# Optimization experiments

Measured on AMD Instinct MI355X. Metric: run time of the kernel, lower is better.

The kernel has to match this reference:

```python
import jax, jax.numpy as jnp
import numpy as np

B, S, H, H2, NH, K, L, V, TOUT, MEL = 16, 256, 384, 1536, 2, 3, 4, 256, 1024, 80


def _ln(x, sb):
    # sb: [2, H] -> (scale, bias)
    m = x.mean(-1, keepdims=True)
    v = x.var(-1, keepdims=True)
    return (x - m) * jax.lax.rsqrt(v + 1e-5) * sb[0] + sb[1]


def _conv1d(x, w, b):
    # x: [B, T, Cin], w: [K, Cin, Cout]
    return jax.lax.conv_general_dilated(x, w, (1,), 'SAME',
                                         dimension_numbers=('NWC', 'WIO', 'NWC')) + b


def _mha(x, w, b):
    # w: [4, H, H] (q, k, v, o), b: [4, H]
    T = x.shape[1]
    dh = H // NH
    q = (x @ w[0] + b[0]).reshape(B, T, NH, dh)
    k = (x @ w[1] + b[1]).reshape(B, T, NH, dh)
    v = (x @ w[2] + b[2]).reshape(B, T, NH, dh)
    s = jnp.einsum('bqhd,bkhd->bhqk', q, k) / np.sqrt(dh).astype(np.float32)
    a = jax.nn.softmax(s, axis=-1)
    o = jnp.einsum('bhqk,bkhd->bqhd', a, v).reshape(B, T, H)
    return o @ w[3] + b[3]


def _fft_block(x, aw, ab, c1w, c1b, c2w, c2b, ln):
    x = _ln(x + _mha(x, aw, ab), ln[0])
    f = _conv1d(jax.nn.relu(_conv1d(x, c1w, c1b)), c2w, c2b)
    return _ln(x + f, ln[1])


def _posenc(x):
    T = x.shape[1]
    pos = jnp.arange(T, dtype=jnp.float32)[:, None]
    den = jnp.exp(-np.log(10000.0) * jnp.arange(0, H, 2, dtype=jnp.float32) / H)
    ang = pos * den[None, :]
    pe = jnp.stack([jnp.sin(ang), jnp.cos(ang)], axis=-1).reshape(T, H)
    return x + pe[None]


def setup_inputs() -> dict:
    key = jax.random.key(0)
    ks = iter(jax.random.split(key, 32))
    sc = 0.02
    inp = {}
    inp['tokens'] = jax.random.randint(next(ks), (B, S), 0, V, dtype=jnp.int32)
    inp['alignes'] = jax.random.randint(next(ks), (B, S), 0, 8).astype(jnp.int64)
    inp['tok_emb'] = jax.random.normal(next(ks), (V, H), jnp.float32) * sc
    for pre in ('enc', 'dec'):
        inp[pre + '_attn_w'] = jax.random.normal(next(ks), (L, 4, H, H), jnp.float32) * sc
        inp[pre + '_attn_b'] = jnp.zeros((L, 4, H), jnp.float32)
        inp[pre + '_conv1_w'] = jax.random.normal(next(ks), (L, K, H, H2), jnp.float32) * sc
        inp[pre + '_conv1_b'] = jnp.zeros((L, H2), jnp.float32)
        inp[pre + '_conv2_w'] = jax.random.normal(next(ks), (L, K, H2, H), jnp.float32) * sc
        inp[pre + '_conv2_b'] = jnp.zeros((L, H), jnp.float32)
        ln = jnp.stack([jnp.ones((L, 2, H)), jnp.zeros((L, 2, H))], axis=2)  # [L,2,2,H]
        inp[pre + '_ln'] = ln.astype(jnp.float32)
    inp['al_conv1_w'] = jax.random.normal(next(ks), (K, H, H), jnp.float32) * sc
    inp['al_conv1_b'] = jnp.zeros((H,), jnp.float32)
    inp['al_conv2_w'] = jax.random.normal(next(ks), (K, H, H), jnp.float32) * sc
    inp['al_conv2_b'] = jnp.zeros((H,), jnp.float32)
    inp['al_ln'] = jnp.stack([jnp.ones((2, H)), jnp.zeros((2, H))], axis=1).astype(jnp.float32)
    inp['al_lin_w'] = jax.random.normal(next(ks), (H, 1), jnp.float32) * sc
    inp['al_lin_b'] = jnp.zeros((1,), jnp.float32)
    inp['dec_lin_w'] = jax.random.normal(next(ks), (H, MEL), jnp.float32) * sc
    inp['dec_lin_b'] = jnp.zeros((MEL,), jnp.float32)
    return inp


def reference(tokens, alignes, tok_emb, enc_attn_w, enc_attn_b, enc_conv1_w,
              enc_conv1_b, enc_conv2_w, enc_conv2_b, enc_ln, dec_attn_w,
              dec_attn_b, dec_conv1_w, dec_conv1_b, dec_conv2_w, dec_conv2_b,
              dec_ln, al_conv1_w, al_conv1_b, al_conv2_w, al_conv2_b, al_ln,
              al_lin_w, al_lin_b, dec_lin_w, dec_lin_b):
    # ---- Encoder ----
    x = tok_emb[tokens] * np.sqrt(H).astype(np.float32)
    x = _posenc(x)
    for i in range(L):
        x = _fft_block(x, enc_attn_w[i], enc_attn_b[i], enc_conv1_w[i],
                       enc_conv1_b[i], enc_conv2_w[i], enc_conv2_b[i], enc_ln[i])
    # ---- Aligner (duration predictor) ----
    h = jax.nn.relu(_conv1d(x, al_conv1_w, al_conv1_b))
    h = _ln(h, al_ln[0])
    h = jax.nn.relu(_conv1d(h, al_conv2_w, al_conv2_b))
    h = _ln(h, al_ln[1])
    length_pred = (h @ al_lin_w + al_lin_b)[..., 0]  # [B, S]
    # ---- Length regulator: repeat_interleave + pad_sequence (static TOUT) ----
    dur = alignes.astype(jnp.int32)
    cum = jnp.cumsum(dur, axis=1)                    # [B, S]
    t = jnp.arange(TOUT, dtype=jnp.int32)
    idx = jax.vmap(lambda c: jnp.searchsorted(c, t, side='right'))(cum)  # [B, TOUT]
    valid = t[None, :] < cum[:, -1:]
    idx = jnp.clip(idx, 0, S - 1)
    expanded = jnp.take_along_axis(x, idx[:, :, None], axis=1)
    expanded = expanded * valid[:, :, None].astype(x.dtype)
    # ---- Decoder ----
    y = _posenc(expanded)
    for i in range(L):
        y = _fft_block(y, dec_attn_w[i], dec_attn_b[i], dec_conv1_w[i],
                       dec_conv1_b[i], dec_conv2_w[i], dec_conv2_b[i], dec_ln[i])
    mel = y @ dec_lin_w + dec_lin_b                  # [B, TOUT, 80]
    return jnp.transpose(mel, (0, 2, 1)), length_pred
```

## Files before the change

### kernel.cpp

```cpp
#include <hip/hip_runtime.h>
#include <cstdint>
#include <cstddef>

#define B_    16
#define S_    256
#define H_    384
#define H2_   1536
#define NH_   2
#define DH_   192
#define TOUT_ 1024
#define MEL_  80
#define L_    4

#define F_BIAS  1
#define F_RES   2
#define F_RELU  4
#define F_STF   8
#define F_STB   16
#define F_TRANS 32

typedef __attribute__((ext_vector_type(8))) short short8;
typedef __attribute__((ext_vector_type(4))) float floatx4;

typedef const __attribute__((address_space(1))) unsigned int* as1p;
typedef __attribute__((address_space(3))) unsigned int* as3p;

__device__ __forceinline__ void gld16(const void* g, void* l) {
  __builtin_amdgcn_global_load_lds((as1p)g, (as3p)l, 16, 0, 0);
}

__device__ __forceinline__ short f2b(float f) {
  union { float f; unsigned u; } v; v.f = f;
  unsigned r = (v.u + 0x7fffu + ((v.u >> 16) & 1u)) >> 16;
  return (short)r;
}

__device__ __forceinline__ float pe_val(int t, int i) {
  int j = i >> 1;
  float den = __expf(-9.210340371976184f * (float)(2 * j) / (float)H_);
  float ang = (float)t * den;
  return (i & 1) ? __cosf(ang) : __sinf(ang);
}

__global__ __launch_bounds__(256) void wtrans_kernel(const float* __restrict__ sa,
                                                     const float* __restrict__ sb,
                                                     int na, int K, int N,
                                                     short* __restrict__ dst) {
  __shared__ float t[32][33];
  int id = blockIdx.z;
  const float* s = (id < na) ? sa + (size_t)id * K * N : sb + (size_t)(id - na) * K * N;
  short* o = dst + (size_t)id * K * N;
  int n0 = blockIdx.x * 32, k0 = blockIdx.y * 32;
  int tx = threadIdx.x & 31, ty = threadIdx.x >> 5;
#pragma unroll
  for (int i = 0; i < 4; ++i)
    t[ty + i * 8][tx] = s[(size_t)(k0 + ty + i * 8) * N + n0 + tx];
  __syncthreads();
#pragma unroll
  for (int i = 0; i < 4; ++i)
    o[(size_t)(n0 + ty + i * 8) * K + k0 + tx] = f2b(t[tx][ty + i * 8]);
}

__global__ void melpad_kernel(const float* __restrict__ w, short* __restrict__ dst) {
  int i = blockIdx.x * 256 + threadIdx.x;
  int n = i / H_, k = i - n * H_;
  dst[i] = (n < MEL_) ? f2b(w[(size_t)k * MEL_ + n]) : (short)0;
}

__global__ void embed_kernel(const int* __restrict__ tokens, const float* __restrict__ emb,
                             float* __restrict__ xf, short* __restrict__ xb) {
  int bs = blockIdx.x;
  int t  = bs & (S_ - 1);
  int tok = tokens[bs];
  const float* e = emb + (size_t)tok * H_;
  float* of = xf + (size_t)bs * H_;
  short* ob = xb + (size_t)bs * H_;
  for (int i = threadIdx.x; i < H_; i += blockDim.x) {
    float v = e[i] * 19.595917942265423f + pe_val(t, i);
    of[i] = v; ob[i] = f2b(v);
  }
}

template<int NTAPS, int MTW>
__global__ __launch_bounds__(256) void mfma_gemm(
    const short* __restrict__ A, const short* __restrict__ Wt,
    const float* __restrict__ bias, const float* __restrict__ res,
    float* __restrict__ Cf, short* __restrict__ Cb, const short* __restrict__ zbuf,
    int M, int N, int Kd, int T, int Nout, int flags)
{
  constexpr int TM   = MTW * 32;
  constexpr int HB   = NTAPS / 2;
  constexpr int RA   = TM + NTAPS - 1;
  constexpr int RNDA = (RA + 63) / 64;
  __shared__ __align__(16) short As[RA * 32];
  __shared__ __align__(16) short Bs[NTAPS * 128 * 32];
  const int tid = threadIdx.x;
  const int wave = tid >> 6, lane = tid & 63, quad = lane >> 4, lm = lane & 15;

  const int nbx = gridDim.x;
  const int lin = blockIdx.y * nbx + blockIdx.x;
  const int xcd = lin & 7, j = lin >> 3;
  const int bx = j % nbx;
  const int by = xcd + 8 * (j / nbx);

  const int bm = by * TM, bn = bx * 128;
  const int wm = (wave >> 1) * (TM / 2), wn = (wave & 1) * 64;
  const int b0 = bm / T, t0 = bm - b0 * T;
  floatx4 acc[MTW][4] = {};

  for (int k0 = 0; k0 < Kd; k0 += 32) {
#pragma unroll
    for (int jj = 0; jj < RNDA; ++jj) {
      int r0 = (jj == RNDA - 1) ? (RA - 64) : jj * 64;
      int r = r0 + (tid >> 2);
      int t = t0 - HB + r;
      const short* g = (t >= 0 && t < T)
          ? (A + (size_t)(b0 * T + t) * Kd + k0 + (tid & 3) * 8) : zbuf;
      gld16(g, As + r0 * 32 + wave * 512);
    }
#pragma unroll
    for (int jj = 0; jj < 2 * NTAPS; ++jj) {
      int gi = jj * 256 + tid;
      int tap = gi >> 9, rr = (gi >> 2) & 127, ch = gi & 3;
      const short* g = Wt + ((size_t)tap * N + bn + rr) * Kd + k0 + ch * 8;
      gld16(g, Bs + jj * 2048 + wave * 512);
    }
    __syncthreads();
#pragma unroll
    for (int tap = 0; tap < NTAPS; ++tap) {
      short8 af[MTW], bfr[4];
#pragma unroll
      for (int mt = 0; mt < MTW; ++mt)
        af[mt] = *(const short8*)(&As[(wm + mt * 16 + lm + tap) * 32 + quad * 8]);
#pragma unroll
      for (int nt = 0; nt < 4; ++nt)
        bfr[nt] = *(const short8*)(&Bs[tap * 4096 + (wn + nt * 16 + lm) * 32 + quad * 8]);
#pragma unroll
      for (int mt = 0; mt < MTW; ++mt)
#pragma unroll
        for (int nt = 0; nt < 4; ++nt)
          acc[mt][nt] = __builtin_amdgcn_mfma_f32_16x16x32_bf16(af[mt], bfr[nt],
                                                                acc[mt][nt], 0, 0, 0);
    }
    __syncthreads();
  }

#pragma unroll
  for (int mt = 0; mt < MTW; ++mt) {
#pragma unroll
    for (int r2 = 0; r2 < 4; ++r2) {
      int gm = bm + wm + mt * 16 + quad * 4 + r2;
#pragma unroll
      for (int nt = 0; nt < 4; ++nt) {
        int gn = bn + wn + nt * 16 + lm;
        float v = acc[mt][nt][r2];
        if (flags & F_TRANS) {
          if (gn < Nout) {
            if (flags & F_BIAS) v += bias[gn];
            int bb = gm / T, tt = gm - bb * T;
            Cf[((size_t)bb * Nout + gn) * T + tt] = v;
          }
          continue;
        }
        if (flags & F_BIAS) v += bias[gn];
        size_t idx = (size_t)gm * N + gn;
        if (flags & F_RES) v += res[idx];
        if (flags & F_RELU) v = fmaxf(v, 0.f);
        if (flags & F_STF) Cf[idx] = v;
        if (flags & F_STB) Cb[idx] = f2b(v);
      }
    }
  }
}

__global__ __launch_bounds__(256) void vtrans_kernel(const short* __restrict__ qkv,
                                                     short* __restrict__ vt, int T) {
  __shared__ short tile[32][34];
  int b = blockIdx.z, d0 = blockIdx.y * 32, t0 = blockIdx.x * 32;
  int tx = threadIdx.x & 31, ty = threadIdx.x >> 5;
#pragma unroll
  for (int i = 0; i < 4; ++i)
    tile[ty + i * 8][tx] = qkv[(size_t)(b * T + t0 + ty + i * 8) * 1152 + 768 + d0 + tx];
  __syncthreads();
  int h = (d0 >= DH_) ? 1 : 0;
  int dd0 = d0 - h * DH_;
#pragma unroll
  for (int i = 0; i < 4; ++i)
    vt[((size_t)((b * NH_ + h) * DH_) + dd0 + ty + i * 8) * T + t0 + tx] = tile[tx][ty + i * 8];
}

template<int T>
__global__ __launch_bounds__(256) void attn_flash(const short* __restrict__ qkv,
                                                  const short* __restrict__ vt,
                                                  short* __restrict__ o)
{
  constexpr int NKT = T / 32;
  __shared__ __align__(16) short Kb[2][6144];
  __shared__ __align__(16) short Vb[2][6144];
  __shared__ __align__(16) short Pb[4][16 * 40];
  const int tid = threadIdx.x;
  const int wave = tid >> 6, lane = tid & 63, quad = lane >> 4, lm = lane & 15;
  const int id = blockIdx.x;
  const int bh = id & 31, h = bh & 1, b = bh >> 1;
  const int q0 = (id >> 5) * 64;
  const short* qb = qkv + (size_t)b * T * 1152 + h * DH_;
  const short* kb = qb + 384;
  const short* vb = vt + (size_t)(b * NH_ + h) * DH_ * T;

  short8 qf[6];
  {
    const short* qrow = qb + (size_t)(q0 + wave * 16 + lm) * 1152 + quad * 8;
#pragma unroll
    for (int c6 = 0; c6 < 6; ++c6) qf[c6] = *(const short8*)(qrow + c6 * 32);
  }

  auto stage = [&](int kc, int bi) {
#pragma unroll
    for (int j = 0; j < 3; ++j) {
      int g = j * 256 + tid;
      int lmg = g & 15, qg = (g >> 4) & 3, ct = g >> 6;
      int c6 = ct % 6, kt = ct / 6;
      gld16(kb + (size_t)(kc * 32 + kt * 16 + lmg) * 1152 + c6 * 32 + qg * 8,
            &Kb[bi][j * 2048 + wave * 512]);
    }
#pragma unroll
    for (int j = 0; j < 3; ++j) {
      int g = j * 256 + tid;
      int lmg = g & 15, qg = (g >> 4) & 3, dt = g >> 6;
      gld16(vb + (size_t)(dt * 16 + lmg) * T + kc * 32 + qg * 8,
            &Vb[bi][j * 2048 + wave * 512]);
    }
  };

  float m_r[4] = {-1e30f, -1e30f, -1e30f, -1e30f};
  float l_r[4] = {0.f, 0.f, 0.f, 0.f};
  floatx4 oacc[12] = {};

  stage(0, 0);
  __syncthreads();

  for (int kc = 0; kc < NKT; ++kc) {
    const int cur = kc & 1;
    if (kc + 1 < NKT) stage(kc + 1, cur ^ 1);

    floatx4 s0 = {0.f, 0.f, 0.f, 0.f}, s1 = {0.f, 0.f, 0.f, 0.f};
#pragma unroll
    for (int c6 = 0; c6 < 6; ++c6) {
      short8 k0f = *(const short8*)(&Kb[cur][(c6 * 64 + quad * 16 + lm) * 8]);
      short8 k1f = *(const short8*)(&Kb[cur][((6 + c6) * 64 + quad * 16 + lm) * 8]);
      s0 = __builtin_amdgcn_mfma_f32_16x16x32_bf16(qf[c6], k0f, s0, 0, 0, 0);
      s1 = __builtin_amdgcn_mfma_f32_16x16x32_bf16(qf[c6], k1f, s1, 0, 0, 0);
    }

    float al[4];
#pragma unroll
    for (int r2 = 0; r2 < 4; ++r2) {
      float a = s0[r2] * 0.07216878364870323f;
      float c = s1[r2] * 0.07216878364870323f;
      float t = fmaxf(a, c);
#pragma unroll
      for (int off = 1; off < 16; off <<= 1) t = fmaxf(t, __shfl_xor(t, off, 64));
      float mn = fmaxf(m_r[r2], t);
      al[r2] = __expf(m_r[r2] - mn);
      m_r[r2] = mn;
      float e0 = __expf(a - mn), e1 = __expf(c - mn);
      l_r[r2] = al[r2] * l_r[r2] + e0 + e1;
      Pb[wave][(quad * 4 + r2) * 40 + lm]      = f2b(e0);
      Pb[wave][(quad * 4 + r2) * 40 + 16 + lm] = f2b(e1);
    }
#pragma unroll
    for (int dt = 0; dt < 12; ++dt) {
#pragma unroll
      for (int r2 = 0; r2 < 4; ++r2) oacc[dt][r2] *= al[r2];
    }

    short8 pf = *(const short8*)(&Pb[wave][lm * 40 + quad * 8]);
#pragma unroll
    for (int dt = 0; dt < 12; ++dt) {
      short8 vf = *(const short8*)(&Vb[cur][(dt * 64 + quad * 16 + lm) * 8]);
      oacc[dt] = __builtin_amdgcn_mfma_f32_16x16x32_bf16(pf, vf, oacc[dt], 0, 0, 0);
    }
    __syncthreads();
  }

#pragma unroll
  for (int r2 = 0; r2 < 4; ++r2) {
#pragma unroll
    for (int off = 1; off < 16; off <<= 1) l_r[r2] += __shfl_xor(l_r[r2], off, 64);
    l_r[r2] = 1.f / l_r[r2];
  }
  short* orow = o + (size_t)(b * T + q0 + wave * 16) * H_ + h * DH_;
#pragma unroll
  for (int dt = 0; dt < 12; ++dt) {
#pragma unroll
    for (int r2 = 0; r2 < 4; ++r2)
      orow[(size_t)(quad * 4 + r2) * H_ + dt * 16 + lm] = f2b(oacc[dt][r2] * l_r[r2]);
  }
}

__global__ __launch_bounds__(256) void ln_kernel(const float* __restrict__ X,
                                                 const float* __restrict__ sb,
                                                 float* __restrict__ Yf,
                                                 short* __restrict__ Yb, int M)
{
  int row  = blockIdx.x * 4 + (threadIdx.x >> 6);
  int lane = threadIdx.x & 63;
  const float* x = X + (size_t)row * H_;
  float v[6]; float s = 0.f, ss = 0.f;
#pragma unroll
  for (int i = 0; i < 6; ++i) { v[i] = x[lane + i * 64]; s += v[i]; ss += v[i] * v[i]; }
#pragma unroll
  for (int o = 32; o; o >>= 1) { s += __shfl_down(s, o, 64); ss += __shfl_down(ss, o, 64); }
  s = __shfl(s, 0, 64); ss = __shfl(ss, 0, 64);
  float mean = s * (1.0f / H_);
  float var  = ss * (1.0f / H_) - mean * mean;
  float r = rsqrtf(var + 1e-5f);
  float* yf = Yf + (size_t)row * H_;
#pragma unroll
  for (int i = 0; i < 6; ++i) {
    int c = lane + i * 64;
    float y = (v[i] - mean) * r * sb[c] + sb[H_ + c];
    yf[c] = y;
    if (Yb) Yb[(size_t)row * H_ + c] = f2b(y);
  }
}

__global__ void gemv_kernel(const float* __restrict__ A, const float* __restrict__ w,
                            const float* __restrict__ bflt, float* __restrict__ out, int M)
{
  int row  = blockIdx.x * 4 + (threadIdx.x >> 6);
  int lane = threadIdx.x & 63;
  const float* a = A + (size_t)row * H_;
  float s = 0.f;
#pragma unroll
  for (int i = 0; i < 6; ++i) s += a[lane + i * 64] * w[lane + i * 64];
#pragma unroll
  for (int o = 32; o; o >>= 1) s += __shfl_down(s, o, 64);
  if (lane == 0) out[row] = s + bflt[0];
}

__global__ void cumsum_kernel(const int* __restrict__ al, int* __restrict__ cum) {
  int b = threadIdx.x;
  if (b < B_) {
    int acc = 0;
    for (int s = 0; s < S_; ++s) { acc += al[b * S_ + s]; cum[b * S_ + s] = acc; }
  }
}

__global__ void expand_kernel(const float* __restrict__ xe, const int* __restrict__ cum,
                              float* __restrict__ yf, short* __restrict__ yb) {
  int t = blockIdx.x, b = blockIdx.y;
  const int* c = cum + b * S_;
  int lo = 0, hi = S_;
  while (lo < hi) { int mid = (lo + hi) >> 1; if (c[mid] <= t) lo = mid + 1; else hi = mid; }
  int idx = lo < S_ ? lo : S_ - 1;
  bool valid = t < c[S_ - 1];
  const float* src = xe + ((size_t)b * S_ + idx) * H_;
  float* df = yf + ((size_t)b * TOUT_ + t) * H_;
  short* db = yb + ((size_t)b * TOUT_ + t) * H_;
  for (int i = threadIdx.x; i < H_; i += blockDim.x) {
    float v = (valid ? src[i] : 0.f) + pe_val(t, i);
    df[i] = v; db[i] = f2b(v);
  }
}

static inline void gemm(const short* A, const short* Wt, const float* bias, const float* res,
                        float* Cf, short* Cb, const short* zbuf, int M, int N, int Kd, int T,
                        int ntaps, int mtw, int Nout, int flags, hipStream_t st) {
  int tm = mtw * 32;
  dim3 g(N / 128, M / tm);
  if (ntaps == 3) {
    if (mtw == 4)
      mfma_gemm<3,4><<<g, 256, 0, st>>>(A, Wt, bias, res, Cf, Cb, zbuf, M, N, Kd, T, Nout, flags);
    else
      mfma_gemm<3,2><<<g, 256, 0, st>>>(A, Wt, bias, res, Cf, Cb, zbuf, M, N, Kd, T, Nout, flags);
  } else {
    if (mtw == 4)
      mfma_gemm<1,4><<<g, 256, 0, st>>>(A, Wt, bias, res, Cf, Cb, zbuf, M, N, Kd, T, Nout, flags);
    else
      mfma_gemm<1,2><<<g, 256, 0, st>>>(A, Wt, bias, res, Cf, Cb, zbuf, M, N, Kd, T, Nout, flags);
  }
}

struct LayerW { const short *attn, *c1, *c2; const float *ab, *c1b, *c2b, *ln; };

static void fft_block(float* x, short* xb, short* qkvb, short* ob, short* vtb, short* h2b,
                      const short* zbuf, const LayerW& w, int T, hipStream_t st)
{
  int M = B_ * T;
  const size_t msz = (size_t)H_ * H_;
  gemm(xb, w.attn, w.ab, nullptr, nullptr, qkvb, zbuf, M, 1152, H_, T, 1, 4, 0,
       F_BIAS | F_STB, st);
  vtrans_kernel<<<dim3(T / 32, 12, B_), 256, 0, st>>>(qkvb, vtb, T);
  if (T == 256) attn_flash<256><<<dim3((256 / 64) * 32), 256, 0, st>>>(qkvb, vtb, ob);
  else          attn_flash<1024><<<dim3((1024 / 64) * 32), 256, 0, st>>>(qkvb, vtb, ob);
  gemm(ob, w.attn + 3 * msz, w.ab + 3 * H_, x, x, nullptr, zbuf, M, H_, H_, T, 1, 2, 0,
       F_BIAS | F_RES | F_STF, st);
  ln_kernel<<<M / 4, 256, 0, st>>>(x, w.ln, x, xb, M);
  gemm(xb, w.c1, w.c1b, nullptr, nullptr, h2b, zbuf, M, H2_, H_, T, 3, 4, 0,
       F_BIAS | F_RELU | F_STB, st);
  gemm(h2b, w.c2, w.c2b, x, x, nullptr, zbuf, M, H_, H2_, T, 3, 2, 0,
       F_BIAS | F_RES | F_STF, st);
  ln_kernel<<<M / 4, 256, 0, st>>>(x, w.ln + 2 * H_, x, xb, M);
}

extern "C" void kernel_launch(void* const* d_in, const int* in_sizes, int n_in,
                              void* d_out, int out_size, void* d_ws, size_t ws_size,
                              hipStream_t stream)
{
  (void)in_sizes; (void)n_in; (void)out_size; (void)ws_size;
  const int*   tokens      = (const int*)d_in[0];
  const int*   alignes     = (const int*)d_in[1];
  const float* tok_emb     = (const float*)d_in[2];
  const float* enc_attn_w  = (const float*)d_in[3];
  const float* enc_attn_b  = (const float*)d_in[4];
  const float* enc_conv1_w = (const float*)d_in[5];
  const float* enc_conv1_b = (const float*)d_in[6];
  const float* enc_conv2_w = (const float*)d_in[7];
  const float* enc_conv2_b = (const float*)d_in[8];
  const float* enc_ln      = (const float*)d_in[9];
  const float* dec_attn_w  = (const float*)d_in[10];
  const float* dec_attn_b  = (const float*)d_in[11];
  const float* dec_conv1_w = (const float*)d_in[12];
  const float* dec_conv1_b = (const float*)d_in[13];
  const float* dec_conv2_w = (const float*)d_in[14];
  const float* dec_conv2_b = (const float*)d_in[15];
  const float* dec_ln      = (const float*)d_in[16];
  const float* al_c1w      = (const float*)d_in[17];
  const float* al_c1b      = (const float*)d_in[18];
  const float* al_c2w      = (const float*)d_in[19];
  const float* al_c2b      = (const float*)d_in[20];
  const float* al_ln       = (const float*)d_in[21];
  const float* al_lin_w    = (const float*)d_in[22];
  const float* al_lin_b    = (const float*)d_in[23];
  const float* dec_lin_w   = (const float*)d_in[24];
  const float* dec_lin_b   = (const float*)d_in[25];

  char* base = (char*)d_ws;
  size_t off = 0;
  auto alloc = [&](size_t bytes) -> char* {
    char* p = base + off;
    off += (bytes + 255) & ~(size_t)255;
    return p;
  };
  const size_t ME = (size_t)B_ * S_;
  const size_t MD = (size_t)B_ * TOUT_;
  float* xe   = (float*)alloc(ME * H_ * 4);
  short* xeb  = (short*)alloc(ME * H_ * 2);
  float* xd   = (float*)alloc(MD * H_ * 4);
  short* xdb  = (short*)alloc(MD * H_ * 2);
  short* qkvb = (short*)alloc(MD * 1152 * 2);
  short* ob   = (short*)alloc(MD * H_ * 2);
  short* h2b  = (short*)alloc(MD * H2_ * 2);
  short* vtb  = h2b;
  short* wAt  = (short*)alloc((size_t)32 * H_ * H_ * 2);
  short* wAl  = (short*)alloc((size_t)6 * H_ * H_ * 2);
  short* wC1  = (short*)alloc((size_t)24 * H_ * H2_ * 2);
  short* wC2  = (short*)alloc((size_t)24 * H_ * H2_ * 2);
  short* wMel = (short*)alloc((size_t)128 * H_ * 2);
  int*   cum  = (int*)alloc(ME * 4);
  short* zbuf = (short*)alloc(256);
  float* alf  = xd;
  short* alb  = xdb;

  float* mel_out = (float*)d_out;
  float* len_out = mel_out + (size_t)B_ * MEL_ * TOUT_;

  hipMemsetAsync(zbuf, 0, 256, stream);

  wtrans_kernel<<<dim3(12, 12, 32), 256, 0, stream>>>(enc_attn_w, dec_attn_w, 16, H_, H_, wAt);
  wtrans_kernel<<<dim3(12, 12, 6),  256, 0, stream>>>(al_c1w, al_c2w, 3, H_, H_, wAl);
  wtrans_kernel<<<dim3(48, 12, 24), 256, 0, stream>>>(enc_conv1_w, dec_conv1_w, 12, H_, H2_, wC1);
  wtrans_kernel<<<dim3(12, 48, 24), 256, 0, stream>>>(enc_conv2_w, dec_conv2_w, 12, H2_, H_, wC2);
  melpad_kernel<<<dim3(128 * H_ / 256), 256, 0, stream>>>(dec_lin_w, wMel);

  embed_kernel<<<dim3(B_ * S_), 128, 0, stream>>>(tokens, tok_emb, xe, xeb);
  for (int i = 0; i < L_; ++i) {
    LayerW w;
    w.attn = wAt + (size_t)i * 4 * H_ * H_;
    w.c1   = wC1 + (size_t)i * 3 * H_ * H2_;
    w.c2   = wC2 + (size_t)i * 3 * H_ * H2_;
    w.ab   = enc_attn_b + (size_t)i * 4 * H_;
    w.c1b  = enc_conv1_b + (size_t)i * H2_;
    w.c2b  = enc_conv2_b + (size_t)i * H_;
    w.ln   = enc_ln + (size_t)i * 4 * H_;
    fft_block(xe, xeb, qkvb, ob, vtb, h2b, zbuf, w, S_, stream);
  }

  {
    int Ma = B_ * S_;
    gemm(xeb, wAl, al_c1b, nullptr, alf, nullptr, zbuf, Ma, H_, H_, S_, 3, 2, 0,
         F_BIAS | F_RELU | F_STF, stream);
    ln_kernel<<<Ma / 4, 256, 0, stream>>>(alf, al_ln, alf, alb, Ma);
    gemm(alb, wAl + (size_t)3 * H_ * H_, al_c2b, nullptr, alf, nullptr, zbuf, Ma, H_, H_, S_,
         3, 2, 0, F_BIAS | F_RELU | F_STF, stream);
    ln_kernel<<<Ma / 4, 256, 0, stream>>>(alf, al_ln + 2 * H_, alf, (short*)nullptr, Ma);
    gemv_kernel<<<Ma / 4, 256, 0, stream>>>(alf, al_lin_w, al_lin_b, len_out, Ma);
  }

  cumsum_kernel<<<1, 64, 0, stream>>>(alignes, cum);
  expand_kernel<<<dim3(TOUT_, B_), 128, 0, stream>>>(xe, cum, xd, xdb);

  for (int i = 0; i < L_; ++i) {
    LayerW w;
    w.attn = wAt + (size_t)(16 + i * 4) * H_ * H_;
    w.c1   = wC1 + (size_t)(12 + i * 3) * H_ * H2_;
    w.c2   = wC2 + (size_t)(12 + i * 3) * H_ * H2_;
    w.ab   = dec_attn_b + (size_t)i * 4 * H_;
    w.c1b  = dec_conv1_b + (size_t)i * H2_;
    w.c2b  = dec_conv2_b + (size_t)i * H_;
    w.ln   = dec_ln + (size_t)i * 4 * H_;
    fft_block(xd, xdb, qkvb, ob, vtb, h2b, zbuf, w, TOUT_, stream);
  }

  gemm(xdb, wMel, dec_lin_b, nullptr, mel_out, nullptr, zbuf, B_ * TOUT_, 128, H_, TOUT_,
       1, 2, MEL_, F_BIAS | F_TRANS, stream);
}
```

Baseline: 3.165 ms.

## Double-buffer A tile in LDS and load weight fragments directly from global

The GEMM/conv kernel now double-buffers the activation tile in shared memory, prefetching the next K slice while computing the current one. Weight fragments are read straight from global memory into registers instead of being staged through LDS. The XCD-aware block swizzle is dropped in favour of plain blockIdx mapping, and the grid width rounds N up. This removes the B-tile LDS traffic and one barrier's worth of latency. In exchange, each wave issues uncoalesced-ish global loads for weights, uses more registers, and loses L2 locality from the swizzle. The prefetch is issued before the compute, but only one barrier remains per iteration.

```diff
diff --git a/kernel.cpp b/kernel.cpp
--- a/kernel.cpp
+++ b/kernel.cpp
@@ -92,23 +92,16 @@
   constexpr int HB   = NTAPS / 2;
   constexpr int RA   = TM + NTAPS - 1;
   constexpr int RNDA = (RA + 63) / 64;
-  __shared__ __align__(16) short As[RA * 32];
-  __shared__ __align__(16) short Bs[NTAPS * 128 * 32];
+  __shared__ __align__(16) short As[2][RA * 32];
   const int tid = threadIdx.x;
   const int wave = tid >> 6, lane = tid & 63, quad = lane >> 4, lm = lane & 15;
-
-  const int nbx = gridDim.x;
-  const int lin = blockIdx.y * nbx + blockIdx.x;
-  const int xcd = lin & 7, j = lin >> 3;
-  const int bx = j % nbx;
-  const int by = xcd + 8 * (j / nbx);
-
-  const int bm = by * TM, bn = bx * 128;
+  const int bm = blockIdx.y * TM, bn = blockIdx.x * 128;
   const int wm = (wave >> 1) * (TM / 2), wn = (wave & 1) * 64;
   const int b0 = bm / T, t0 = bm - b0 * T;
+  const int NK = Kd >> 5;
   floatx4 acc[MTW][4] = {};
 
-  for (int k0 = 0; k0 < Kd; k0 += 32) {
+  auto stageA = [&](int k0, int bi) {
 #pragma unroll
     for (int jj = 0; jj < RNDA; ++jj) {
       int r0 = (jj == RNDA - 1) ? (RA - 64) : jj * 64;
@@ -116,30 +109,34 @@
       int t = t0 - HB + r;
       const short* g = (t >= 0 && t < T)
           ? (A + (size_t)(b0 * T + t) * Kd + k0 + (tid & 3) * 8) : zbuf;
-      gld16(g, As + r0 * 32 + wave * 512);
-    }
-#pragma unroll
-    for (int jj = 0; jj < 2 * NTAPS; ++jj) {
-      int gi = jj * 256 + tid;
-      int tap = gi >> 9, rr = (gi >> 2) & 127, ch = gi & 3;
-      const short* g = Wt + ((size_t)tap * N + bn + rr) * Kd + k0 + ch * 8;
-      gld16(g, Bs + jj * 2048 + wave * 512);
-    }
-    __syncthreads();
+      gld16(g, &As[bi][r0 * 32] + wave * 512);
+    }
+  };
+
+  stageA(0, 0);
+  __syncthreads();
+
+  for (int i = 0; i < NK; ++i) {
+    const int k0 = i << 5, bi = i & 1;
+    if (i + 1 < NK) stageA(k0 + 32, bi ^ 1);
+    short8 bfr[NTAPS][4];
+#pragma unroll
+    for (int tap = 0; tap < NTAPS; ++tap)
+#pragma unroll
+      for (int nt = 0; nt < 4; ++nt)
+        bfr[tap][nt] = *(const short8*)(Wt + ((size_t)tap * N + bn + wn + nt * 16 + lm) * Kd
+                                        + k0 + quad * 8);
 #pragma unroll
     for (int tap = 0; tap < NTAPS; ++tap) {
-      short8 af[MTW], bfr[4];
+      short8 af[MTW];
 #pragma unroll
       for (int mt = 0; mt < MTW; ++mt)
-        af[mt] = *(const short8*)(&As[(wm + mt * 16 + lm + tap) * 32 + quad * 8]);
-#pragma unroll
-      for (int nt = 0; nt < 4; ++nt)
-        bfr[nt] = *(const short8*)(&Bs[tap * 4096 + (wn + nt * 16 + lm) * 32 + quad * 8]);
+        af[mt] = *(const short8*)(&As[bi][(wm + mt * 16 + lm + tap) * 32 + quad * 8]);
 #pragma unroll
       for (int mt = 0; mt < MTW; ++mt)
 #pragma unroll
         for (int nt = 0; nt < 4; ++nt)
-          acc[mt][nt] = __builtin_amdgcn_mfma_f32_16x16x32_bf16(af[mt], bfr[nt],
+          acc[mt][nt] = __builtin_amdgcn_mfma_f32_16x16x32_bf16(af[mt], bfr[tap][nt],
                                                                 acc[mt][nt], 0, 0, 0);
     }
     __syncthreads();
@@ -368,7 +365,7 @@
                         float* Cf, short* Cb, const short* zbuf, int M, int N, int Kd, int T,
                         int ntaps, int mtw, int Nout, int flags, hipStream_t st) {
   int tm = mtw * 32;
-  dim3 g(N / 128, M / tm);
+  dim3 g((N + 127) / 128, M / tm);
   if (ntaps == 3) {
     if (mtw == 4)
       mfma_gemm<3,4><<<g, 256, 0, st>>>(A, Wt, bias, res, Cf, Cb, zbuf, M, N, Kd, T, Nout, flags);
```

Result: slower. 3.635 ms (+14.8%).
